# Kernel tuning notes

Hardware: AMD Instinct MI355X
Metric: run time of the kernel (lower is better)

The kernel has to match this reference:

```python
import jax, jax.numpy as jnp
import numpy as np

HIDDEN = 64
NUM_LAYERS = 3
EPS = 1e-5


def setup_inputs() -> dict:
    key = jax.random.key(0)
    ks = jax.random.split(key, 16)
    N, E, F_IN, H, C = 100000, 3200000, 12, HIDDEN, 2
    x = jax.random.normal(ks[0], (N, F_IN), dtype=jnp.float32)
    edge_index = jax.random.randint(ks[1], (2, E), 0, N, dtype=jnp.int64)
    s = lambda k, sh, fan: jax.random.normal(k, sh, dtype=jnp.float32) / np.sqrt(fan)
    return {
        "x": x,
        "edge_index": edge_index,
        "W_in": s(ks[2], (F_IN, H), F_IN),
        "b_in": jnp.zeros((H,), jnp.float32),
        "W_g": s(ks[3], (NUM_LAYERS, H, H), H),
        "b_g": jnp.zeros((NUM_LAYERS, H), jnp.float32),
        "gamma": jnp.ones((NUM_LAYERS, H), jnp.float32),
        "beta": jnp.zeros((NUM_LAYERS, H), jnp.float32),
        "W_c1": s(ks[4], (H, H // 2), H),
        "b_c1": jnp.zeros((H // 2,), jnp.float32),
        "W_c2": s(ks[5], (H // 2, C), H // 2),
        "b_c2": jnp.zeros((C,), jnp.float32),
    }


def _gcn_norm(edge_index, N):
    # GCNConv default: add self loops, symmetric normalization D^-1/2 (A+I) D^-1/2
    src, dst = edge_index[0], edge_index[1]
    deg = jax.ops.segment_sum(jnp.ones_like(dst, jnp.float32), dst, num_segments=N) + 1.0
    dinv = jax.lax.rsqrt(deg)
    norm_e = dinv[src] * dinv[dst]          # [E] per-edge coefficient
    self_norm = dinv * dinv                 # [N] self-loop coefficient
    return src, dst, norm_e, self_norm


def _gcn_layer(h, W, b, src, dst, norm_e, self_norm, N):
    h = h @ W                                # [N, H] linear transform first
    agg = jax.ops.segment_sum(h[src] * norm_e[:, None], dst, num_segments=N)
    return agg + h * self_norm[:, None] + b


def _batchnorm(h, gamma, beta):
    mu = jnp.mean(h, axis=0)
    var = jnp.mean(jnp.square(h - mu), axis=0)  # biased, as torch BN
    return (h - mu) * jax.lax.rsqrt(var + EPS) * gamma + beta


def reference(x, edge_index, W_in, b_in, W_g, b_g, gamma, beta, W_c1, b_c1, W_c2, b_c2):
    N = x.shape[0]
    src, dst, norm_e, self_norm = _gcn_norm(edge_index, N)
    h = jax.nn.relu(x @ W_in + b_in)
    for i in range(NUM_LAYERS):
        h = _gcn_layer(h, W_g[i], b_g[i], src, dst, norm_e, self_norm, N)
        h = _batchnorm(h, gamma[i], beta[i])
        if i < NUM_LAYERS - 1:
            h = jax.nn.relu(h)  # dropout omitted (inference/deterministic)
    h = jax.nn.relu(h @ W_c1 + b_c1)
    return h @ W_c2 + b_c2
```

## Files before the change

### kernel.cpp

```cpp
#include <hip/hip_runtime.h>

#define EPSV 1e-5f
#define BSH 8
#define BSZ 256
#define PCOLS 104

__device__ inline float blo(unsigned u) { return __uint_as_float(u << 16); }
__device__ inline float bhi(unsigned u) { return __uint_as_float(u & 0xFFFF0000u); }
__device__ inline unsigned rne16(float v) {
    unsigned u = __float_as_uint(v);
    return (u + 0x7FFFu + ((u >> 16) & 1u)) >> 16;
}
__device__ inline unsigned pk(float lo, float hi) {
    return (rne16(hi) << 16) | rne16(lo);
}


__global__ __launch_bounds__(256) void k_hist(const int* __restrict__ dst,
                                              int* __restrict__ bcount, int E) {
    __shared__ int hist[1024];
    int t = threadIdx.x;
#pragma unroll
    for (int i = 0; i < 4; i++) hist[t + 256 * i] = 0;
    __syncthreads();
    int e0 = blockIdx.x * 4096;
#pragma unroll
    for (int r = 0; r < 16; r++) {
        int e = e0 + r * 256 + t;
        if (e < E) atomicAdd(&hist[dst[e] >> BSH], 1);
    }
    __syncthreads();
#pragma unroll
    for (int i = 0; i < 4; i++) {
        int bk = t + 256 * i;
        int h = hist[bk];
        if (h) atomicAdd(&bcount[bk], h);
    }
}

__global__ __launch_bounds__(256) void k_bscan(const int* __restrict__ bcount,
                                               int* __restrict__ bstart,
                                               int* __restrict__ gcur, int NB) {
    int t = threadIdx.x;
    int base = t * 4;
    int c[4], s = 0;
#pragma unroll
    for (int i = 0; i < 4; i++) {
        c[i] = (base + i < NB) ? bcount[base + i] : 0;
        s += c[i];
    }
    __shared__ int ls[256];
    ls[t] = s;
    __syncthreads();
    for (int off = 1; off < 256; off <<= 1) {
        int x = (t >= off) ? ls[t - off] : 0;
        __syncthreads();
        ls[t] += x;
        __syncthreads();
    }
    int run = (t == 0) ? 0 : ls[t - 1];
#pragma unroll
    for (int i = 0; i < 4; i++) {
        bstart[base + i] = run;
        gcur[base + i] = run;
        run += c[i];
    }
    if (t == 255) bstart[1024] = ls[255];
}

__global__ __launch_bounds__(256) void k_split(const int* __restrict__ src,
                                               const int* __restrict__ dst,
                                               int* __restrict__ gcur,
                                               unsigned* __restrict__ pairs, int E) {
    __shared__ int hist[1024];
    __shared__ int gb[1024];
    int t = threadIdx.x;
    int e0 = blockIdx.x * 4096;
    int sreg[16], dreg[16];
#pragma unroll
    for (int i = 0; i < 4; i++) hist[t + 256 * i] = 0;
    __syncthreads();
#pragma unroll
    for (int r = 0; r < 16; r++) {
        int e = e0 + r * 256 + t;
        if (e < E) {
            sreg[r] = src[e];
            dreg[r] = dst[e];
            atomicAdd(&hist[dreg[r] >> BSH], 1);
        } else {
            dreg[r] = -1;
        }
    }
    __syncthreads();
#pragma unroll
    for (int i = 0; i < 4; i++) {
        int bk = t + 256 * i;
        int h = hist[bk];
        gb[bk] = h ? atomicAdd(&gcur[bk], h) : 0;
    }
    __syncthreads();
#pragma unroll
    for (int i = 0; i < 4; i++) hist[t + 256 * i] = 0;
    __syncthreads();
#pragma unroll
    for (int r = 0; r < 16; r++) {
        if (dreg[r] >= 0) {
            int bk = dreg[r] >> BSH;
            int rk = atomicAdd(&hist[bk], 1);
            pairs[gb[bk] + rk] = ((unsigned)(dreg[r] & (BSZ - 1)) << 22) |
                                 (unsigned)sreg[r];
        }
    }
}

__global__ __launch_bounds__(256) void k_build(const unsigned* __restrict__ pairs,
                                               const int* __restrict__ bstart,
                                               int* __restrict__ rowptr,
                                               int* __restrict__ rowend,
                                               float* __restrict__ dinv,
                                               int* __restrict__ colidx, int N) {
    int bid = blockIdx.x, t = threadIdx.x;
    int n0 = bid << BSH;
    int e0 = bstart[bid], e1 = bstart[bid + 1];
    __shared__ int cnt[256];
    __shared__ int ls[256];
    __shared__ int cur[256];
    cnt[t] = 0;
    __syncthreads();
    for (int e = e0 + t; e < e1; e += 256)
        atomicAdd(&cnt[pairs[e] >> 22], 1);
    __syncthreads();
    ls[t] = cnt[t];
    __syncthreads();
    for (int off = 1; off < 256; off <<= 1) {
        int x = (t >= off) ? ls[t - off] : 0;
        __syncthreads();
        ls[t] += x;
        __syncthreads();
    }
    int start = e0 + ((t == 0) ? 0 : ls[t - 1]);
    cur[t] = start;
    int node = n0 + t;
    if (node < N) {
        rowptr[node] = start;
        rowend[node] = start + cnt[t];
        dinv[node] = rsqrtf((float)cnt[t] + 1.0f);
    }
    __syncthreads();
    for (int e = e0 + t; e < e1; e += 256) {
        unsigned p = pairs[e];
        int r = atomicAdd(&cur[p >> 22], 1);
        colidx[r] = (int)(p & 0x3FFFFFu);
    }
}


__global__ __launch_bounds__(256) void k_gemm0(const float* __restrict__ x,
                                               const float* __restrict__ Win,
                                               const float* __restrict__ bin,
                                               const float* __restrict__ W,
                                               const float* __restrict__ dinv,
                                               unsigned short* __restrict__ hl, int N) {
    __shared__ float zbuf[4][64];
    int wv = threadIdx.x >> 6;
    int j = threadIdx.x & 63;
    float w[64];
#pragma unroll
    for (int k = 0; k < 64; k++) w[k] = W[k * 64 + j];
    float wi[12];
#pragma unroll
    for (int k = 0; k < 12; k++) wi[k] = Win[k * 64 + j];
    float bj = bin[j];
    const float4* zr = (const float4*)&zbuf[wv][0];
    int wave = (blockIdx.x * 256 + threadIdx.x) >> 6;
    int nw = (gridDim.x * 256) >> 6;
    for (int node = wave; node < N; node += nw) {
        const float* xr = x + node * 12;
        float z = bj;
#pragma unroll
        for (int k = 0; k < 12; k++) z = fmaf(xr[k], wi[k], z);
        zbuf[wv][j] = fmaxf(z, 0.0f);
        asm volatile("s_waitcnt lgkmcnt(0)" ::: "memory");
        float acc = 0.0f;
#pragma unroll
        for (int kk = 0; kk < 16; kk++) {
            float4 z4 = zr[kk];
            acc = fmaf(z4.x, w[4 * kk + 0], acc);
            acc = fmaf(z4.y, w[4 * kk + 1], acc);
            acc = fmaf(z4.z, w[4 * kk + 2], acc);
            acc = fmaf(z4.w, w[4 * kk + 3], acc);
        }
        hl[node * 64 + j] = (unsigned short)rne16(acc * dinv[node]);
    }
}

__global__ __launch_bounds__(256) void k_gemmn(const float* __restrict__ W,
                                               const float* __restrict__ ab,
                                               const float* __restrict__ dinv,
                                               const unsigned* __restrict__ h2,
                                               unsigned short* __restrict__ hl, int N) {
    __shared__ float zbuf[4][64];
    int wv = threadIdx.x >> 6;
    int j = threadIdx.x & 63;
    float w[64];
#pragma unroll
    for (int k = 0; k < 64; k++) w[k] = W[k * 64 + j];
    float Aj = ab[j], Bj = ab[64 + j];
    const float4* zr = (const float4*)&zbuf[wv][0];
    int wave = (blockIdx.x * 256 + threadIdx.x) >> 6;
    int nw = (gridDim.x * 256) >> 6;
    for (int node = wave; node < N; node += nw) {
        unsigned u = h2[node * 32 + (j >> 1)];
        float h = (j & 1) ? bhi(u) : blo(u);
        zbuf[wv][j] = fmaxf(fmaf(Aj, h, Bj), 0.0f);
        asm volatile("s_waitcnt lgkmcnt(0)" ::: "memory");
        float acc = 0.0f;
#pragma unroll
        for (int kk = 0; kk < 16; kk++) {
            float4 z4 = zr[kk];
            acc = fmaf(z4.x, w[4 * kk + 0], acc);
            acc = fmaf(z4.y, w[4 * kk + 1], acc);
            acc = fmaf(z4.z, w[4 * kk + 2], acc);
            acc = fmaf(z4.w, w[4 * kk + 3], acc);
        }
        hl[node * 64 + j] = (unsigned short)rne16(acc * dinv[node]);
    }
}

__global__ __launch_bounds__(256) void k_agg(const int* __restrict__ rowptr,
                                             const int* __restrict__ rowend,
                                             const int* __restrict__ colidx,
                                             const float* __restrict__ dinv,
                                             const unsigned* __restrict__ hl2,
                                             const float* __restrict__ b,
                                             unsigned* __restrict__ out2,
                                             float* __restrict__ ps, int N) {
    __shared__ float sms[8][64];
    __shared__ float smq[8][64];
    int t = threadIdx.x;
    int hw = t >> 5;
    int lane = t & 31;
    int sub = lane >> 3;
    int q = lane & 7;
    const uint4* H = (const uint4*)hl2;
    int fb = q * 8;
    float bb0 = b[fb + 0], bb1 = b[fb + 1], bb2 = b[fb + 2], bb3 = b[fb + 3];
    float bb4 = b[fb + 4], bb5 = b[fb + 5], bb6 = b[fb + 6], bb7 = b[fb + 7];

    float s0 = 0.f, s1 = 0.f, s2 = 0.f, s3 = 0.f;
    float s4 = 0.f, s5 = 0.f, s6 = 0.f, s7 = 0.f;
    float q0 = 0.f, q1 = 0.f, q2 = 0.f, q3 = 0.f;
    float q4 = 0.f, q5 = 0.f, q6 = 0.f, q7 = 0.f;

    int nHW = gridDim.x * 8;
    for (int d = blockIdx.x * 8 + hw; d < N; d += nHW) {
        int e0 = rowptr[d], e1 = rowend[d];

        float a0 = 0.f, a1 = 0.f, a2 = 0.f, a3 = 0.f;
        float a4 = 0.f, a5 = 0.f, a6 = 0.f, a7 = 0.f;
        float b0 = 0.f, b1 = 0.f, b2 = 0.f, b3 = 0.f;
        float b4 = 0.f, b5 = 0.f, b6 = 0.f, b7 = 0.f;
        float c0 = 0.f, c1 = 0.f, c2 = 0.f, c3 = 0.f;
        float c4 = 0.f, c5 = 0.f, c6 = 0.f, c7 = 0.f;
        float g0 = 0.f, g1 = 0.f, g2 = 0.f, g3 = 0.f;
        float g4 = 0.f, g5 = 0.f, g6 = 0.f, g7 = 0.f;

        if (sub == 0) {
            uint4 su = H[d * 8 + q];
            a0 = blo(su.x); a1 = bhi(su.x);
            a2 = blo(su.y); a3 = bhi(su.y);
            a4 = blo(su.z); a5 = bhi(su.z);
            a6 = blo(su.w); a7 = bhi(su.w);
        }

        int e = e0 + sub;
        for (; e + 12 < e1; e += 16) {
            int i0 = colidx[e], i1 = colidx[e + 4];
            int i2 = colidx[e + 8], i3 = colidx[e + 12];
            uint4 u0 = H[i0 * 8 + q], u1 = H[i1 * 8 + q];
            uint4 u2 = H[i2 * 8 + q], u3 = H[i3 * 8 + q];
            a0 += blo(u0.x); a1 += bhi(u0.x); a2 += blo(u0.y); a3 += bhi(u0.y);
            a4 += blo(u0.z); a5 += bhi(u0.z); a6 += blo(u0.w); a7 += bhi(u0.w);
            b0 += blo(u1.x); b1 += bhi(u1.x); b2 += blo(u1.y); b3 += bhi(u1.y);
            b4 += blo(u1.z); b5 += bhi(u1.z); b6 += blo(u1.w); b7 += bhi(u1.w);
            c0 += blo(u2.x); c1 += bhi(u2.x); c2 += blo(u2.y); c3 += bhi(u2.y);
            c4 += blo(u2.z); c5 += bhi(u2.z); c6 += blo(u2.w); c7 += bhi(u2.w);
            g0 += blo(u3.x); g1 += bhi(u3.x); g2 += blo(u3.y); g3 += bhi(u3.y);
            g4 += blo(u3.z); g5 += bhi(u3.z); g6 += blo(u3.w); g7 += bhi(u3.w);
        }
        for (; e < e1; e += 4) {
            uint4 u = H[colidx[e] * 8 + q];
            a0 += blo(u.x); a1 += bhi(u.x); a2 += blo(u.y); a3 += bhi(u.y);
            a4 += blo(u.z); a5 += bhi(u.z); a6 += blo(u.w); a7 += bhi(u.w);
        }
        a0 += (b0 + c0) + g0; a1 += (b1 + c1) + g1;
        a2 += (b2 + c2) + g2; a3 += (b3 + c3) + g3;
        a4 += (b4 + c4) + g4; a5 += (b5 + c5) + g5;
        a6 += (b6 + c6) + g6; a7 += (b7 + c7) + g7;

        a0 += __shfl_xor(a0, 8);  a0 += __shfl_xor(a0, 16);
        a1 += __shfl_xor(a1, 8);  a1 += __shfl_xor(a1, 16);
        a2 += __shfl_xor(a2, 8);  a2 += __shfl_xor(a2, 16);
        a3 += __shfl_xor(a3, 8);  a3 += __shfl_xor(a3, 16);
        a4 += __shfl_xor(a4, 8);  a4 += __shfl_xor(a4, 16);
        a5 += __shfl_xor(a5, 8);  a5 += __shfl_xor(a5, 16);
        a6 += __shfl_xor(a6, 8);  a6 += __shfl_xor(a6, 16);
        a7 += __shfl_xor(a7, 8);  a7 += __shfl_xor(a7, 16);

        if (sub == 0) {
            float dv = dinv[d];
            float o0 = fmaf(a0, dv, bb0);
            float o1 = fmaf(a1, dv, bb1);
            float o2 = fmaf(a2, dv, bb2);
            float o3 = fmaf(a3, dv, bb3);
            float o4 = fmaf(a4, dv, bb4);
            float o5 = fmaf(a5, dv, bb5);
            float o6 = fmaf(a6, dv, bb6);
            float o7 = fmaf(a7, dv, bb7);
            uint4 o;
            o.x = pk(o0, o1);
            o.y = pk(o2, o3);
            o.z = pk(o4, o5);
            o.w = pk(o6, o7);
            ((uint4*)out2)[d * 8 + q] = o;
            s0 += o0; q0 = fmaf(o0, o0, q0);
            s1 += o1; q1 = fmaf(o1, o1, q1);
            s2 += o2; q2 = fmaf(o2, o2, q2);
            s3 += o3; q3 = fmaf(o3, o3, q3);
            s4 += o4; q4 = fmaf(o4, o4, q4);
            s5 += o5; q5 = fmaf(o5, o5, q5);
            s6 += o6; q6 = fmaf(o6, o6, q6);
            s7 += o7; q7 = fmaf(o7, o7, q7);
        }
    }

    if (sub == 0) {
        sms[hw][fb + 0] = s0; sms[hw][fb + 1] = s1;
        sms[hw][fb + 2] = s2; sms[hw][fb + 3] = s3;
        sms[hw][fb + 4] = s4; sms[hw][fb + 5] = s5;
        sms[hw][fb + 6] = s6; sms[hw][fb + 7] = s7;
        smq[hw][fb + 0] = q0; smq[hw][fb + 1] = q1;
        smq[hw][fb + 2] = q2; smq[hw][fb + 3] = q3;
        smq[hw][fb + 4] = q4; smq[hw][fb + 5] = q5;
        smq[hw][fb + 6] = q6; smq[hw][fb + 7] = q7;
    }
    __syncthreads();
    if (t < 64) {
        float S = 0.f, Q = 0.f;
#pragma unroll
        for (int h = 0; h < 8; h++) {
            S += sms[h][t];
            Q += smq[h][t];
        }
        int col = blockIdx.x % PCOLS;
        atomicAdd(&ps[t * PCOLS + col], S);
        atomicAdd(&ps[(64 + t) * PCOLS + col], Q);
    }
}

__global__ __launch_bounds__(64) void k_red(const float* __restrict__ ps,
                                            const float* __restrict__ gamma,
                                            const float* __restrict__ beta,
                                            float* __restrict__ ab, float invN) {
    int t = threadIdx.x;
    float S = 0.f, Q = 0.f;
    for (int i = 0; i < PCOLS; i++) {
        S += ps[t * PCOLS + i];
        Q += ps[(64 + t) * PCOLS + i];
    }
    float mu = S * invN;
    float var = fmaf(-mu, mu, Q * invN);
    float A = rsqrtf(var + EPSV) * gamma[t];
    ab[t] = A;
    ab[64 + t] = fmaf(-mu, A, beta[t]);
}

__global__ __launch_bounds__(256) void k_cls(const unsigned* __restrict__ h2,
                                             const float* __restrict__ ab,
                                             const float* __restrict__ W1,
                                             const float* __restrict__ b1,
                                             const float* __restrict__ W2,
                                             const float* __restrict__ b2,
                                             float* __restrict__ out, int N) {
    int lane = threadIdx.x & 63;
    int half = lane >> 5, jj = lane & 31;
    float w[64];
    float bj = b1[jj];
#pragma unroll
    for (int k = 0; k < 64; k++) {
        float w1 = W1[k * 32 + jj];
        w[k] = ab[k] * w1;
        bj = fmaf(ab[64 + k], w1, bj);
    }
    float w20 = W2[jj * 2 + 0], w21 = W2[jj * 2 + 1];
    float b20 = b2[0], b21 = b2[1];
    int wave = (blockIdx.x * 256 + threadIdx.x) >> 6;
    int nw = (gridDim.x * 256) >> 6;
    for (int base = wave * 2; base < N; base += nw * 2) {
        int node = base + half;
        int vnode = node < N ? node : 0;
        const uint4* row = (const uint4*)(h2 + vnode * 32);
        float acc = bj;
#pragma unroll
        for (int kk = 0; kk < 8; kk++) {
            uint4 u = row[kk];
            acc = fmaf(blo(u.x), w[8 * kk + 0], acc);
            acc = fmaf(bhi(u.x), w[8 * kk + 1], acc);
            acc = fmaf(blo(u.y), w[8 * kk + 2], acc);
            acc = fmaf(bhi(u.y), w[8 * kk + 3], acc);
            acc = fmaf(blo(u.z), w[8 * kk + 4], acc);
            acc = fmaf(bhi(u.z), w[8 * kk + 5], acc);
            acc = fmaf(blo(u.w), w[8 * kk + 6], acc);
            acc = fmaf(bhi(u.w), w[8 * kk + 7], acc);
        }
        float hv = fmaxf(acc, 0.0f);
        float t0 = hv * w20, t1 = hv * w21;
#pragma unroll
        for (int m = 1; m <= 16; m <<= 1) {
            t0 += __shfl_xor(t0, m, 64);
            t1 += __shfl_xor(t1, m, 64);
        }
        if (jj == 0 && node < N) {
            ((float2*)out)[node] = make_float2(t0 + b20, t1 + b21);
        }
    }
}

extern "C" void kernel_launch(void* const* d_in, const int* in_sizes, int n_in,
                              void* d_out, int out_size, void* d_ws, size_t ws_size,
                              hipStream_t stream) {
    const float* x     = (const float*)d_in[0];
    const int*   ei    = (const int*)d_in[1];
    const float* Win   = (const float*)d_in[2];
    const float* bin   = (const float*)d_in[3];
    const float* Wg    = (const float*)d_in[4];
    const float* bg    = (const float*)d_in[5];
    const float* gamma = (const float*)d_in[6];
    const float* beta  = (const float*)d_in[7];
    const float* W1    = (const float*)d_in[8];
    const float* b1    = (const float*)d_in[9];
    const float* W2    = (const float*)d_in[10];
    const float* b2    = (const float*)d_in[11];
    float* out = (float*)d_out;

    int N = in_sizes[0] / 12;
    int E = in_sizes[1] / 2;
    const int* src = ei;
    const int* dst = ei + E;
    float invN = 1.0f / (float)N;
    int NB = (N + BSZ - 1) >> BSH;

    char* ws = (char*)d_ws;
    size_t szhin = ((size_t)N * 64 * 2 + 255) / 256 * 256;
    size_t szE4  = ((size_t)E * 4 + 255) / 256 * 256;
    size_t szN4  = ((size_t)N * 4 + 255) / 256 * 256;
    size_t szps  = (size_t)128 * PCOLS * 4;

    size_t off = 0;
    unsigned* hin2     = (unsigned*)(ws + off); off += szhin;
    unsigned short* hl = (unsigned short*)(ws + off); off += szhin;
    int* colidx        = (int*)(ws + off); off += szE4;
    int* rowptr        = (int*)(ws + off); off += szN4;
    int* rowend        = (int*)(ws + off); off += szN4;
    float* dinv        = (float*)(ws + off); off += szN4;
    int* bcount        = (int*)(ws + off); off += 4096;
    float* ps          = (float*)(ws + off); off += 3 * szps;
    size_t msz = 4096 + 3 * szps;
    int* bstart        = (int*)(ws + off); off += 8192;
    int* gcur          = (int*)(ws + off); off += 4096;
    float* ab          = (float*)(ws + off); off += 512;

    unsigned* pairs = (unsigned*)ws;
    size_t need = off;
    if (2 * szhin < (size_t)E * 4) {
        pairs = (unsigned*)(ws + off);
        need += (size_t)E * 4;
    }
    if (ws_size < need || NB > 1024 || N >= (1 << 22)) return;

    hipMemsetAsync(bcount, 0, msz, stream);

    int EB = (E + 4095) / 4096;
    k_hist<<<EB, 256, 0, stream>>>(dst, bcount, E);
    k_bscan<<<1, 256, 0, stream>>>(bcount, bstart, gcur, NB);
    k_split<<<EB, 256, 0, stream>>>(src, dst, gcur, pairs, E);
    k_build<<<NB, 256, 0, stream>>>(pairs, bstart, rowptr, rowend, dinv, colidx, N);

    int AB = (N + 7) / 8;
    if (AB > 2048) AB = 2048;
    for (int i = 0; i < 3; i++) {
        if (i == 0)
            k_gemm0<<<2048, 256, 0, stream>>>(x, Win, bin, Wg, dinv, hl, N);
        else
            k_gemmn<<<2048, 256, 0, stream>>>(Wg + i * 64 * 64, ab, dinv, hin2,
                                              hl, N);
        k_agg<<<AB, 256, 0, stream>>>(rowptr, rowend, colidx, dinv,
                                      (const unsigned*)hl, bg + i * 64, hin2,
                                      ps + (size_t)i * 128 * PCOLS, N);
        k_red<<<1, 64, 0, stream>>>(ps + (size_t)i * 128 * PCOLS, gamma + i * 64,
                                    beta + i * 64, ab, invN);
    }
    k_cls<<<1024, 256, 0, stream>>>(hin2, ab, W1, b1, W2, b2, out, N);
}
```

Baseline: 512.3 us.

## Split BN statistics into separate pass; fold reduction into consumer kernels

```diff
diff --git a/kernel.cpp b/kernel.cpp
--- a/kernel.cpp
+++ b/kernel.cpp
@@ -3,7 +3,7 @@
 #define EPSV 1e-5f
 #define BSH 8
 #define BSZ 256
-#define PCOLS 104
+#define SB 104
 
 __device__ inline float blo(unsigned u) { return __uint_as_float(u << 16); }
 __device__ inline float bhi(unsigned u) { return __uint_as_float(u & 0xFFFF0000u); }
@@ -195,19 +195,40 @@
 }
 
 __global__ __launch_bounds__(256) void k_gemmn(const float* __restrict__ W,
-                                               const float* __restrict__ ab,
+                                               const float* __restrict__ part,
+                                               const float* __restrict__ gamma,
+                                               const float* __restrict__ beta,
                                                const float* __restrict__ dinv,
                                                const unsigned* __restrict__ h2,
-                                               unsigned short* __restrict__ hl, int N) {
+                                               unsigned short* __restrict__ hl,
+                                               int N, float invN) {
+    __shared__ float abl[128];
+    __shared__ float sq[128];
     __shared__ float zbuf[4][64];
-    int wv = threadIdx.x >> 6;
-    int j = threadIdx.x & 63;
+    int t = threadIdx.x;
+    if (t < 128) {
+        float S = 0.f;
+        for (int i = 0; i < SB; i++) S += part[i * 128 + t];
+        sq[t] = S;
+    }
+    __syncthreads();
+    if (t < 64) {
+        float mu = sq[t] * invN;
+        float var = fmaf(-mu, mu, sq[64 + t] * invN);
+        float A = rsqrtf(var + EPSV) * gamma[t];
+        abl[t] = A;
+        abl[64 + t] = fmaf(-mu, A, beta[t]);
+    }
+    __syncthreads();
+
+    int wv = t >> 6;
+    int j = t & 63;
     float w[64];
 #pragma unroll
     for (int k = 0; k < 64; k++) w[k] = W[k * 64 + j];
-    float Aj = ab[j], Bj = ab[64 + j];
+    float Aj = abl[j], Bj = abl[64 + j];
     const float4* zr = (const float4*)&zbuf[wv][0];
-    int wave = (blockIdx.x * 256 + threadIdx.x) >> 6;
+    int wave = (blockIdx.x * 256 + t) >> 6;
     int nw = (gridDim.x * 256) >> 6;
     for (int node = wave; node < N; node += nw) {
         unsigned u = h2[node * 32 + (j >> 1)];
@@ -233,168 +254,153 @@
                                              const float* __restrict__ dinv,
                                              const unsigned* __restrict__ hl2,
                                              const float* __restrict__ b,
-                                             unsigned* __restrict__ out2,
-                                             float* __restrict__ ps, int N) {
-    __shared__ float sms[8][64];
-    __shared__ float smq[8][64];
+                                             unsigned* __restrict__ out2, int N) {
     int t = threadIdx.x;
     int hw = t >> 5;
     int lane = t & 31;
     int sub = lane >> 3;
     int q = lane & 7;
+    int d = blockIdx.x * 8 + hw;
+    if (d >= N) return;
+    int e0 = rowptr[d], e1 = rowend[d];
     const uint4* H = (const uint4*)hl2;
-    int fb = q * 8;
-    float bb0 = b[fb + 0], bb1 = b[fb + 1], bb2 = b[fb + 2], bb3 = b[fb + 3];
-    float bb4 = b[fb + 4], bb5 = b[fb + 5], bb6 = b[fb + 6], bb7 = b[fb + 7];
-
-    float s0 = 0.f, s1 = 0.f, s2 = 0.f, s3 = 0.f;
-    float s4 = 0.f, s5 = 0.f, s6 = 0.f, s7 = 0.f;
-    float q0 = 0.f, q1 = 0.f, q2 = 0.f, q3 = 0.f;
-    float q4 = 0.f, q5 = 0.f, q6 = 0.f, q7 = 0.f;
-
-    int nHW = gridDim.x * 8;
-    for (int d = blockIdx.x * 8 + hw; d < N; d += nHW) {
-        int e0 = rowptr[d], e1 = rowend[d];
-
-        float a0 = 0.f, a1 = 0.f, a2 = 0.f, a3 = 0.f;
-        float a4 = 0.f, a5 = 0.f, a6 = 0.f, a7 = 0.f;
-        float b0 = 0.f, b1 = 0.f, b2 = 0.f, b3 = 0.f;
-        float b4 = 0.f, b5 = 0.f, b6 = 0.f, b7 = 0.f;
-        float c0 = 0.f, c1 = 0.f, c2 = 0.f, c3 = 0.f;
-        float c4 = 0.f, c5 = 0.f, c6 = 0.f, c7 = 0.f;
-        float g0 = 0.f, g1 = 0.f, g2 = 0.f, g3 = 0.f;
-        float g4 = 0.f, g5 = 0.f, g6 = 0.f, g7 = 0.f;
-
-        if (sub == 0) {
-            uint4 su = H[d * 8 + q];
-            a0 = blo(su.x); a1 = bhi(su.x);
-            a2 = blo(su.y); a3 = bhi(su.y);
-            a4 = blo(su.z); a5 = bhi(su.z);
-            a6 = blo(su.w); a7 = bhi(su.w);
-        }
-
-        int e = e0 + sub;
-        for (; e + 12 < e1; e += 16) {
-            int i0 = colidx[e], i1 = colidx[e + 4];
-            int i2 = colidx[e + 8], i3 = colidx[e + 12];
-            uint4 u0 = H[i0 * 8 + q], u1 = H[i1 * 8 + q];
-            uint4 u2 = H[i2 * 8 + q], u3 = H[i3 * 8 + q];
-            a0 += blo(u0.x); a1 += bhi(u0.x); a2 += blo(u0.y); a3 += bhi(u0.y);
-            a4 += blo(u0.z); a5 += bhi(u0.z); a6 += blo(u0.w); a7 += bhi(u0.w);
-            b0 += blo(u1.x); b1 += bhi(u1.x); b2 += blo(u1.y); b3 += bhi(u1.y);
-            b4 += blo(u1.z); b5 += bhi(u1.z); b6 += blo(u1.w); b7 += bhi(u1.w);
-            c0 += blo(u2.x); c1 += bhi(u2.x); c2 += blo(u2.y); c3 += bhi(u2.y);
-            c4 += blo(u2.z); c5 += bhi(u2.z); c6 += blo(u2.w); c7 += bhi(u2.w);
-            g0 += blo(u3.x); g1 += bhi(u3.x); g2 += blo(u3.y); g3 += bhi(u3.y);
-            g4 += blo(u3.z); g5 += bhi(u3.z); g6 += blo(u3.w); g7 += bhi(u3.w);
-        }
-        for (; e < e1; e += 4) {
-            uint4 u = H[colidx[e] * 8 + q];
-            a0 += blo(u.x); a1 += bhi(u.x); a2 += blo(u.y); a3 += bhi(u.y);
-            a4 += blo(u.z); a5 += bhi(u.z); a6 += blo(u.w); a7 += bhi(u.w);
-        }
-        a0 += (b0 + c0) + g0; a1 += (b1 + c1) + g1;
-        a2 += (b2 + c2) + g2; a3 += (b3 + c3) + g3;
-        a4 += (b4 + c4) + g4; a5 += (b5 + c5) + g5;
-        a6 += (b6 + c6) + g6; a7 += (b7 + c7) + g7;
-
-        a0 += __shfl_xor(a0, 8);  a0 += __shfl_xor(a0, 16);
-        a1 += __shfl_xor(a1, 8);  a1 += __shfl_xor(a1, 16);
-        a2 += __shfl_xor(a2, 8);  a2 += __shfl_xor(a2, 16);
-        a3 += __shfl_xor(a3, 8);  a3 += __shfl_xor(a3, 16);
-        a4 += __shfl_xor(a4, 8);  a4 += __shfl_xor(a4, 16);
-        a5 += __shfl_xor(a5, 8);  a5 += __shfl_xor(a5, 16);
-        a6 += __shfl_xor(a6, 8);  a6 += __shfl_xor(a6, 16);
-        a7 += __shfl_xor(a7, 8);  a7 += __shfl_xor(a7, 16);
-
-        if (sub == 0) {
-            float dv = dinv[d];
-            float o0 = fmaf(a0, dv, bb0);
-            float o1 = fmaf(a1, dv, bb1);
-            float o2 = fmaf(a2, dv, bb2);
-            float o3 = fmaf(a3, dv, bb3);
-            float o4 = fmaf(a4, dv, bb4);
-            float o5 = fmaf(a5, dv, bb5);
-            float o6 = fmaf(a6, dv, bb6);
-            float o7 = fmaf(a7, dv, bb7);
-            uint4 o;
-            o.x = pk(o0, o1);
-            o.y = pk(o2, o3);
-            o.z = pk(o4, o5);
-            o.w = pk(o6, o7);
-            ((uint4*)out2)[d * 8 + q] = o;
-            s0 += o0; q0 = fmaf(o0, o0, q0);
-            s1 += o1; q1 = fmaf(o1, o1, q1);
-            s2 += o2; q2 = fmaf(o2, o2, q2);
-            s3 += o3; q3 = fmaf(o3, o3, q3);
-            s4 += o4; q4 = fmaf(o4, o4, q4);
-            s5 += o5; q5 = fmaf(o5, o5, q5);
-            s6 += o6; q6 = fmaf(o6, o6, q6);
-            s7 += o7; q7 = fmaf(o7, o7, q7);
-        }
-    }
+
+    float a0 = 0.f, a1 = 0.f, a2 = 0.f, a3 = 0.f;
+    float a4 = 0.f, a5 = 0.f, a6 = 0.f, a7 = 0.f;
+    float b0 = 0.f, b1 = 0.f, b2 = 0.f, b3 = 0.f;
+    float b4 = 0.f, b5 = 0.f, b6 = 0.f, b7 = 0.f;
+    float c0 = 0.f, c1 = 0.f, c2 = 0.f, c3 = 0.f;
+    float c4 = 0.f, c5 = 0.f, c6 = 0.f, c7 = 0.f;
+    float g0 = 0.f, g1 = 0.f, g2 = 0.f, g3 = 0.f;
+    float g4 = 0.f, g5 = 0.f, g6 = 0.f, g7 = 0.f;
 
     if (sub == 0) {
-        sms[hw][fb + 0] = s0; sms[hw][fb + 1] = s1;
-        sms[hw][fb + 2] = s2; sms[hw][fb + 3] = s3;
-        sms[hw][fb + 4] = s4; sms[hw][fb + 5] = s5;
-        sms[hw][fb + 6] = s6; sms[hw][fb + 7] = s7;
-        smq[hw][fb + 0] = q0; smq[hw][fb + 1] = q1;
-        smq[hw][fb + 2] = q2; smq[hw][fb + 3] = q3;
-        smq[hw][fb + 4] = q4; smq[hw][fb + 5] = q5;
-        smq[hw][fb + 6] = q6; smq[hw][fb + 7] = q7;
-    }
-    __syncthreads();
-    if (t < 64) {
-        float S = 0.f, Q = 0.f;
-#pragma unroll
-        for (int h = 0; h < 8; h++) {
-            S += sms[h][t];
-            Q += smq[h][t];
-        }
-        int col = blockIdx.x % PCOLS;
-        atomicAdd(&ps[t * PCOLS + col], S);
-        atomicAdd(&ps[(64 + t) * PCOLS + col], Q);
-    }
-}
-
-__global__ __launch_bounds__(64) void k_red(const float* __restrict__ ps,
-                                            const float* __restrict__ gamma,
-                                            const float* __restrict__ beta,
-                                            float* __restrict__ ab, float invN) {
-    int t = threadIdx.x;
-    float S = 0.f, Q = 0.f;
-    for (int i = 0; i < PCOLS; i++) {
-        S += ps[t * PCOLS + i];
-        Q += ps[(64 + t) * PCOLS + i];
-    }
-    float mu = S * invN;
-    float var = fmaf(-mu, mu, Q * invN);
-    float A = rsqrtf(var + EPSV) * gamma[t];
-    ab[t] = A;
-    ab[64 + t] = fmaf(-mu, A, beta[t]);
+        uint4 su = H[d * 8 + q];
+        a0 = blo(su.x); a1 = bhi(su.x);
+        a2 = blo(su.y); a3 = bhi(su.y);
+        a4 = blo(su.z); a5 = bhi(su.z);
+        a6 = blo(su.w); a7 = bhi(su.w);
+    }
+
+    int e = e0 + sub;
+    for (; e + 12 < e1; e += 16) {
+        int s0 = colidx[e], s1 = colidx[e + 4];
+        int s2 = colidx[e + 8], s3 = colidx[e + 12];
+        uint4 u0 = H[s0 * 8 + q], u1 = H[s1 * 8 + q];
+        uint4 u2 = H[s2 * 8 + q], u3 = H[s3 * 8 + q];
+        a0 += blo(u0.x); a1 += bhi(u0.x); a2 += blo(u0.y); a3 += bhi(u0.y);
+        a4 += blo(u0.z); a5 += bhi(u0.z); a6 += blo(u0.w); a7 += bhi(u0.w);
+        b0 += blo(u1.x); b1 += bhi(u1.x); b2 += blo(u1.y); b3 += bhi(u1.y);
+        b4 += blo(u1.z); b5 += bhi(u1.z); b6 += blo(u1.w); b7 += bhi(u1.w);
+        c0 += blo(u2.x); c1 += bhi(u2.x); c2 += blo(u2.y); c3 += bhi(u2.y);
+        c4 += blo(u2.z); c5 += bhi(u2.z); c6 += blo(u2.w); c7 += bhi(u2.w);
+        g0 += blo(u3.x); g1 += bhi(u3.x); g2 += blo(u3.y); g3 += bhi(u3.y);
+        g4 += blo(u3.z); g5 += bhi(u3.z); g6 += blo(u3.w); g7 += bhi(u3.w);
+    }
+    for (; e < e1; e += 4) {
+        uint4 u = H[colidx[e] * 8 + q];
+        a0 += blo(u.x); a1 += bhi(u.x); a2 += blo(u.y); a3 += bhi(u.y);
+        a4 += blo(u.z); a5 += bhi(u.z); a6 += blo(u.w); a7 += bhi(u.w);
+    }
+    a0 += (b0 + c0) + g0; a1 += (b1 + c1) + g1;
+    a2 += (b2 + c2) + g2; a3 += (b3 + c3) + g3;
+    a4 += (b4 + c4) + g4; a5 += (b5 + c5) + g5;
+    a6 += (b6 + c6) + g6; a7 += (b7 + c7) + g7;
+
+    a0 += __shfl_xor(a0, 8);  a0 += __shfl_xor(a0, 16);
+    a1 += __shfl_xor(a1, 8);  a1 += __shfl_xor(a1, 16);
+    a2 += __shfl_xor(a2, 8);  a2 += __shfl_xor(a2, 16);
+    a3 += __shfl_xor(a3, 8);  a3 += __shfl_xor(a3, 16);
+    a4 += __shfl_xor(a4, 8);  a4 += __shfl_xor(a4, 16);
+    a5 += __shfl_xor(a5, 8);  a5 += __shfl_xor(a5, 16);
+    a6 += __shfl_xor(a6, 8);  a6 += __shfl_xor(a6, 16);
+    a7 += __shfl_xor(a7, 8);  a7 += __shfl_xor(a7, 16);
+
+    if (sub == 0) {
+        float dv = dinv[d];
+        int fb = q * 8;
+        float o0 = fmaf(a0, dv, b[fb + 0]);
+        float o1 = fmaf(a1, dv, b[fb + 1]);
+        float o2 = fmaf(a2, dv, b[fb + 2]);
+        float o3 = fmaf(a3, dv, b[fb + 3]);
+        float o4 = fmaf(a4, dv, b[fb + 4]);
+        float o5 = fmaf(a5, dv, b[fb + 5]);
+        float o6 = fmaf(a6, dv, b[fb + 6]);
+        float o7 = fmaf(a7, dv, b[fb + 7]);
+        uint4 o;
+        o.x = pk(o0, o1);
+        o.y = pk(o2, o3);
+        o.z = pk(o4, o5);
+        o.w = pk(o6, o7);
+        ((uint4*)out2)[d * 8 + q] = o;
+    }
+}
+
+__global__ __launch_bounds__(256) void k_stats(const unsigned* __restrict__ h2,
+                                               float* __restrict__ part, int N) {
+    int t = threadIdx.x;
+    int hw = t >> 5, f = t & 31;
+    float s0 = 0.f, s1 = 0.f, q0 = 0.f, q1 = 0.f;
+    for (int node = blockIdx.x * 8 + hw; node < N; node += gridDim.x * 8) {
+        unsigned u = h2[node * 32 + f];
+        float r0 = blo(u), r1 = bhi(u);
+        s0 += r0; q0 = fmaf(r0, r0, q0);
+        s1 += r1; q1 = fmaf(r1, r1, q1);
+    }
+    __shared__ float rs[8][64];
+    __shared__ float rq[8][64];
+    rs[hw][2 * f] = s0; rs[hw][2 * f + 1] = s1;
+    rq[hw][2 * f] = q0; rq[hw][2 * f + 1] = q1;
+    __syncthreads();
+    if (t < 128) {
+        float acc = 0.f;
+#pragma unroll
+        for (int h = 0; h < 8; h++) acc += (t < 64) ? rs[h][t] : rq[h][t - 64];
+        part[blockIdx.x * 128 + t] = acc;
+    }
 }
 
 __global__ __launch_bounds__(256) void k_cls(const unsigned* __restrict__ h2,
-                                             const float* __restrict__ ab,
+                                             const float* __restrict__ part,
+                                             const float* __restrict__ gamma,
+                                             const float* __restrict__ beta,
                                              const float* __restrict__ W1,
                                              const float* __restrict__ b1,
                                              const float* __restrict__ W2,
                                              const float* __restrict__ b2,
-                                             float* __restrict__ out, int N) {
-    int lane = threadIdx.x & 63;
+                                             float* __restrict__ out,
+                                             int N, float invN) {
+    __shared__ float abl[128];
+    __shared__ float sq[128];
+    int t = threadIdx.x;
+    if (t < 128) {
+        float S = 0.f;
+        for (int i = 0; i < SB; i++) S += part[i * 128 + t];
+        sq[t] = S;
+    }
+    __syncthreads();
+    if (t < 64) {
+        float mu = sq[t] * invN;
+        float var = fmaf(-mu, mu, sq[64 + t] * invN);
+        float A = rsqrtf(var + EPSV) * gamma[t];
+        abl[t] = A;
+        abl[64 + t] = fmaf(-mu, A, beta[t]);
+    }
+    __syncthreads();
+
+    int lane = t & 63;
     int half = lane >> 5, jj = lane & 31;
     float w[64];
     float bj = b1[jj];
 #pragma unroll
     for (int k = 0; k < 64; k++) {
         float w1 = W1[k * 32 + jj];
-        w[k] = ab[k] * w1;
-        bj = fmaf(ab[64 + k], w1, bj);
+        w[k] = abl[k] * w1;
+        bj = fmaf(abl[64 + k], w1, bj);
     }
     float w20 = W2[jj * 2 + 0], w21 = W2[jj * 2 + 1];
     float b20 = b2[0], b21 = b2[1];
-    int wave = (blockIdx.x * 256 + threadIdx.x) >> 6;
+    int wave = (blockIdx.x * 256 + t) >> 6;
     int nw = (gridDim.x * 256) >> 6;
     for (int base = wave * 2; base < N; base += nw * 2) {
         int node = base + half;
@@ -454,7 +460,6 @@
     size_t szhin = ((size_t)N * 64 * 2 + 255) / 256 * 256;
     size_t szE4  = ((size_t)E * 4 + 255) / 256 * 256;
     size_t szN4  = ((size_t)N * 4 + 255) / 256 * 256;
-    size_t szps  = (size_t)128 * PCOLS * 4;
 
     size_t off = 0;
     unsigned* hin2     = (unsigned*)(ws + off); off += szhin;
@@ -464,11 +469,9 @@
     int* rowend        = (int*)(ws + off); off += szN4;
     float* dinv        = (float*)(ws + off); off += szN4;
     int* bcount        = (int*)(ws + off); off += 4096;
-    float* ps          = (float*)(ws + off); off += 3 * szps;
-    size_t msz = 4096 + 3 * szps;
     int* bstart        = (int*)(ws + off); off += 8192;
     int* gcur          = (int*)(ws + off); off += 4096;
-    float* ab          = (float*)(ws + off); off += 512;
+    float* part        = (float*)(ws + off); off += (size_t)SB * 128 * 4;
 
     unsigned* pairs = (unsigned*)ws;
     size_t need = off;
@@ -478,7 +481,7 @@
     }
     if (ws_size < need || NB > 1024 || N >= (1 << 22)) return;
 
-    hipMemsetAsync(bcount, 0, msz, stream);
+    hipMemsetAsync(bcount, 0, 4096, stream);
 
     int EB = (E + 4095) / 4096;
     k_hist<<<EB, 256, 0, stream>>>(dst, bcount, E);
@@ -487,18 +490,18 @@
     k_build<<<NB, 256, 0, stream>>>(pairs, bstart, rowptr, rowend, dinv, colidx, N);
 
     int AB = (N + 7) / 8;
-    if (AB > 2048) AB = 2048;
     for (int i = 0; i < 3; i++) {
         if (i == 0)
             k_gemm0<<<2048, 256, 0, stream>>>(x, Win, bin, Wg, dinv, hl, N);
         else
-            k_gemmn<<<2048, 256, 0, stream>>>(Wg + i * 64 * 64, ab, dinv, hin2,
-                                              hl, N);
+            k_gemmn<<<2048, 256, 0, stream>>>(Wg + i * 64 * 64, part,
+                                              gamma + (i - 1) * 64,
+                                              beta + (i - 1) * 64, dinv, hin2,
+                                              hl, N, invN);
         k_agg<<<AB, 256, 0, stream>>>(rowptr, rowend, colidx, dinv,
-                                      (const unsigned*)hl, bg + i * 64, hin2,
-                                      ps + (size_t)i * 128 * PCOLS, N);
-        k_red<<<1, 64, 0, stream>>>(ps + (size_t)i * 128 * PCOLS, gamma + i * 64,
-                                    beta + i * 64, ab, invN);
-    }
-    k_cls<<<1024, 256, 0, stream>>>(hin2, ab, W1, b1, W2, b2, out, N);
-}
+                                      (const unsigned*)hl, bg + i * 64, hin2, N);
+        k_stats<<<SB, 256, 0, stream>>>(hin2, part, N);
+    }
+    k_cls<<<1024, 256, 0, stream>>>(hin2, part, gamma + 128, beta + 128,
+                                    W1, b1, W2, b2, out, N, invN);
+}
```

New measurement: 569.2 us. 11.1% more time.
